# Optimization experiments

Measured on AMD Instinct MI355X. Metric: run time of the kernel, lower is better.

The kernel has to match this reference:

```python
import jax, jax.numpy as jnp
import numpy as np

CLAMP = 2.0
SPLIT1 = 48  # split_len1 (channels - channels//2)


def _down(x):
    # pixel-unshuffle: equivalent to the grouped stride-2 conv with 0/1 kernels
    B, C, H, W = x.shape
    x = x.reshape(B, C, H // 2, 2, W // 2, 2)
    x = x.transpose(0, 1, 3, 5, 2, 4)  # (B, C, di, dj, H/2, W/2)
    return x.reshape(B, C * 4, H // 2, W // 2)


def _conv(x, w, b, stride):
    y = jax.lax.conv_general_dilated(
        x, w, window_strides=(stride, stride), padding=[(1, 1), (1, 1)],
        dimension_numbers=('NCHW', 'OIHW', 'NCHW'))
    return y + b[None, :, None, None]


def _affine(x, a):
    # forward affine coupling: x * exp(clamp*tanh(0.2*a_s)) + a_t
    ch = x.shape[1]
    sub_jac = CLAMP * jnp.tanh(0.2 * a[:, :ch])
    return x * jnp.exp(sub_jac) + a[:, ch:]


def setup_inputs() -> dict:
    key = jax.random.key(0)
    ks = jax.random.split(key, 4)
    B, C, H, W = 32, 96, 64, 64
    s1, s2 = SPLIT1, C - SPLIT1
    x = jax.random.normal(ks[0], (B, C, H, W), jnp.float32)
    # s_hi: strided 3x3 conv, split_len1 -> 8*split_len2
    w_hi = jax.random.normal(ks[1], (8 * s2, s1, 3, 3), jnp.float32) * 0.05
    b_hi = jnp.zeros((8 * s2,), jnp.float32)
    # s_lo: same-res 3x3 conv, 4*split_len2 -> 8*split_len1
    w_lo = jax.random.normal(ks[2], (8 * s1, 4 * s2, 3, 3), jnp.float32) * 0.05
    b_lo = jnp.zeros((8 * s1,), jnp.float32)
    # actnorm params: act_norm init = 10.0 * 1.0 (SOFTPLUS branch)
    ch4 = 4 * C
    act_norm = jnp.full((1, ch4, 1, 1), 10.0, jnp.float32)
    act_offset = jnp.zeros((1, ch4, 1, 1), jnp.float32)
    # hard permutation matrix (permute_soft=False), fixed seed
    rng = np.random.default_rng(0)
    perm = rng.permutation(ch4)
    pw = np.zeros((ch4, ch4), np.float32)
    pw[np.arange(ch4), perm] = 1.0
    perm_w = jnp.asarray(pw)
    return dict(x=x, w_hi=w_hi, b_hi=b_hi, w_lo=w_lo, b_lo=b_lo,
                act_norm=act_norm, act_offset=act_offset, perm_w=perm_w)


def reference(x, w_hi, b_hi, w_lo, b_lo, act_norm, act_offset, perm_w):
    x1, x2 = x[:, :SPLIT1], x[:, SPLIT1:]
    y2 = _down(x2)                     # (B, 4*s2, H/2, W/2)
    a1 = _conv(x1, w_hi, b_hi, 2)      # (B, 8*s2, H/2, W/2)
    y2 = _affine(y2, a1)
    y1 = _down(x1)                     # (B, 4*s1, H/2, W/2)
    a2 = _conv(y2, w_lo, b_lo, 1)      # (B, 8*s1, H/2, W/2)
    y1 = _affine(y1, a2)
    out = jnp.concatenate([y1, y2], axis=1)  # (B, 4*C, H/2, W/2)
    # actnorm (SOFTPLUS: 0.1 * softplus_{beta=0.5}) + hard 1x1 permutation
    scale = 0.2 * jax.nn.softplus(0.5 * act_norm)
    out = jnp.einsum('bchw,oc->bohw', out * scale + act_offset, perm_w)
    return out
```

## Files before the change

kernel.cpp:

```cpp
#include <hip/hip_runtime.h>
#include <hip/hip_bf16.h>

typedef __attribute__((ext_vector_type(8))) short s16x8;
typedef __attribute__((ext_vector_type(4))) short s16x4;
typedef __attribute__((ext_vector_type(4))) float f32x4;
typedef unsigned short u16;

#define WS_FWD    0
#define WS_INV    2048
#define WS_SCALE  4096
#define WS_OFFS   6144
#define WS_WHI    8192
#define WS_XD     2097152
#define WS_WLO    14680064
#define WS_Y2     16777216

static __device__ __forceinline__ u16 f2bf(float f) {
    __hip_bfloat16 h = __float2bfloat16(f);
    return *reinterpret_cast<u16*>(&h);
}
static __device__ __forceinline__ float bf2f(u16 u) {
    __hip_bfloat16 h = *reinterpret_cast<__hip_bfloat16*>(&u);
    return __bfloat162float(h);
}

static __device__ __forceinline__ void gl_lds16(const void* g, void* l) {
    __builtin_amdgcn_global_load_lds(
        (const __attribute__((address_space(1))) unsigned int*)g,
        (__attribute__((address_space(3))) unsigned int*)l, 16, 0, 0);
}


__global__ __launch_bounds__(256)
void k_setup(const float* __restrict__ pw, const float* __restrict__ an,
             const float* __restrict__ ao, const float* __restrict__ w_hi,
             const float* __restrict__ w_lo, int* __restrict__ fwd,
             int* __restrict__ inv, float* __restrict__ scale,
             float* __restrict__ offs, u16* __restrict__ whi,
             u16* __restrict__ wlo)
{
    const int blk = blockIdx.x;
    const int tid = threadIdx.x;
    if (blk < 2592) {
        int gid = blk * 256 + tid;
        int c32 = gid & 31;
        int n   = (gid >> 5) % 384;
        int tkc = gid / (384 * 32);
        int kc  = tkc % 6;
        int t   = tkc / 6;
        int c   = kc * 32 + c32;
        wlo[gid] = f2bf(w_lo[((size_t)n * 192 + c) * 9 + t]);
    } else if (blk < 3744) {
        int gid = (blk - 2592) * 256 + tid;
        int c32 = gid & 31;
        int n   = (gid >> 5) % 384;
        int tkc = gid / (384 * 32);
        int kc  = tkc % 6;
        int t   = tkc / 6;
        int c   = kc * 32 + c32;
        int th = t >> 1, tw = t & 1;
        int cin = c >> 2, dy = (c >> 1) & 1, dx = c & 1;
        float wv = 0.f;
        if (!(th == 0 && dy == 0) && !(tw == 0 && dx == 0)) {
            int ky = (th == 0) ? 0 : 1 + dy;
            int kx = (tw == 0) ? 0 : 1 + dx;
            wv = w_hi[(((size_t)n * 48 + cin) * 3 + ky) * 3 + kx];
        }
        whi[gid] = f2bf(wv);
    } else {
        int gid = (blk - 3744) * 256 + tid;
        int o = gid / 384;
        int c = gid - o * 384;
        if (pw[gid] > 0.5f) { fwd[o] = c; inv[c] = o; }
        if (gid < 384) {
            scale[gid] = 0.2f * log1pf(expf(0.5f * an[gid]));
            offs[gid]  = ao[gid];
        }
    }
}

__global__ __launch_bounds__(256)
void k_xd(const float* __restrict__ x, u16* __restrict__ xd)
{
    int gid = blockIdx.x * 256 + threadIdx.x;
    int pix = gid / 48;
    int j = gid - pix * 48;
    int b = pix >> 10, h = (pix >> 5) & 31, w = pix & 31;
    const float* xp = &x[(((size_t)b * 96 + j) * 64 + 2 * h) * 64 + 2 * w];
    float2 r0 = *(const float2*)xp;
    float2 r1 = *(const float2*)(xp + 64);
    int c0 = j * 4;
    int g = c0 >> 3;
    size_t off = ((size_t)b * 32 + h) * 6144 + w * 192 + ((g ^ (w & 7)) << 3) + (c0 & 7);
    s16x4 v;
    v[0] = (short)f2bf(r0.x); v[1] = (short)f2bf(r0.y);
    v[2] = (short)f2bf(r1.x); v[3] = (short)f2bf(r1.y);
    *(s16x4*)&xd[off] = v;
}

template <int T>
__global__ __launch_bounds__(256)
void f_gemm(const u16* __restrict__ in_t, const u16* __restrict__ wpk,
            const float* __restrict__ bias, const float* __restrict__ x,
            const int* __restrict__ inv, const float* __restrict__ scale,
            const float* __restrict__ offs, u16* __restrict__ y2out,
            float* __restrict__ out)
{
    const int tid = threadIdx.x;
    const int lane = tid & 63;
    const int wave = tid >> 6;
    const int l16 = lane & 15;
    const int quad = lane >> 4;
    const int mblk = blockIdx.x;
    const int b = mblk >> 4;
    const int h0 = (mblk & 15) << 1;
    const int n0 = wave * 96;

    __shared__ u16 sm[384 * 68];

    const s16x8 zero8 = {0, 0, 0, 0, 0, 0, 0, 0};
    for (int r = 0; r < 4; ++r) {
        int ih = h0 - 1 + r;
        if (ih >= 0 && ih < 32) {
            const char* gsrc = (const char*)in_t + ((size_t)b * 32 + ih) * 12288;
#pragma unroll
            for (int j = 0; j < 3; ++j) {
                int off = j * 4096 + tid * 16;
                gl_lds16(gsrc + off, (char*)sm + r * 12288 + off);
            }
        } else {
#pragma unroll
            for (int j = 0; j < 3; ++j)
                *(s16x8*)((char*)sm + r * 12288 + j * 4096 + tid * 16) = zero8;
        }
    }
    __syncthreads();

    const f32x4 zero4 = {0.f, 0.f, 0.f, 0.f};
    f32x4 acc[4][6];
#pragma unroll
    for (int a = 0; a < 4; ++a)
#pragma unroll
        for (int c = 0; c < 6; ++c) acc[a][c] = zero4;

    for (int t = 0; t < T; ++t) {
        const int dh = (T == 4) ? ((t >> 1) - 1) : (t / 3 - 1);
        const int dw = (T == 4) ? ((t & 1) - 1) : (t % 3 - 1);
#pragma unroll
        for (int kc = 0; kc < 6; ++kc) {
            const u16* wp = wpk + ((size_t)(t * 6 + kc) * 384) * 32;
            s16x8 bf[6];
#pragma unroll
            for (int ns = 0; ns < 6; ++ns)
                bf[ns] = *(const s16x8*)(wp + (n0 + ns * 16 + l16) * 32 + quad * 8);
            const int g = kc * 4 + quad;
            s16x8 af[4];
#pragma unroll
            for (int ms = 0; ms < 4; ++ms) {
                int m = ms * 16 + l16;
                int r = (m >> 5) + dh + 1;
                int iw = (m & 31) + dw;
                int iwc = iw < 0 ? 0 : (iw > 31 ? 31 : iw);
                s16x8 v = *(const s16x8*)&sm[r * 6144 + iwc * 192 + ((g ^ (iwc & 7)) << 3)];
                if (iw != iwc) v = zero8;
                af[ms] = v;
            }
#pragma unroll
            for (int ms = 0; ms < 4; ++ms)
#pragma unroll
                for (int ns = 0; ns < 6; ++ns)
                    acc[ms][ns] = __builtin_amdgcn_mfma_f32_16x16x32_bf16(
                        af[ms], bf[ns], acc[ms][ns], 0, 0, 0);
        }
    }

    __syncthreads();

#pragma unroll
    for (int ms = 0; ms < 4; ++ms) {
#pragma unroll
        for (int ns = 0; ns < 6; ++ns) {
            int n = n0 + ns * 16 + l16;
            float bv = bias[n];
            s16x4 pk;
#pragma unroll
            for (int r4 = 0; r4 < 4; ++r4)
                pk[r4] = (short)f2bf(acc[ms][ns][r4] + bv);
            *(s16x4*)&sm[n * 68 + ms * 16 + quad * 4] = pk;
        }
    }
    __syncthreads();

    {
        const int m = lane;
        const int h = h0 + (m >> 5);
        const int w = m & 31;
        for (int i = 0; i < 48; ++i) {
            int c = wave * 48 + i;
            float a_s = bf2f(sm[c * 68 + m]);
            float a_o = bf2f(sm[(c + 192) * 68 + m]);
            int cin = (T == 4 ? 48 : 0) + (c >> 2);
            float xv = x[(((size_t)b * 96 + cin) * 64 + (2 * h + ((c >> 1) & 1))) * 64
                         + (2 * w + (c & 1))];
            float e = expf(0.4f * a_s);
            float sj = 2.f - 4.f / (e + 1.f);
            float y = xv * expf(sj) + a_o;
            int cg = (T == 4) ? (192 + c) : c;
            int o = inv[cg];
            if (T == 4) {
                u16 yb = f2bf(y);
                sm[c * 68 + m] = yb;
                out[(((size_t)b * 384 + o) * 32 + h) * 32 + w] =
                    bf2f(yb) * scale[cg] + offs[cg];
            } else {
                out[(((size_t)b * 384 + o) * 32 + h) * 32 + w] =
                    y * scale[cg] + offs[cg];
            }
        }
    }

    if (T == 4) {
        __syncthreads();
        for (int it = 0; it < 6; ++it) {
            int v = it * 256 + tid;
            int m2 = v / 24;
            int c8 = v - m2 * 24;
            int c0 = c8 * 8;
            int h2 = h0 + (m2 >> 5);
            int w2 = m2 & 31;
            s16x8 yv;
#pragma unroll
            for (int j = 0; j < 8; ++j)
                yv[j] = (short)sm[(c0 + j) * 68 + m2];
            size_t off = ((size_t)b * 32 + h2) * 6144 + w2 * 192 + ((c8 ^ (w2 & 7)) << 3);
            *(s16x8*)&y2out[off] = yv;
        }
    }
}

extern "C" void kernel_launch(void* const* d_in, const int* in_sizes, int n_in,
                              void* d_out, int out_size, void* d_ws, size_t ws_size,
                              hipStream_t stream)
{
    const float* x        = (const float*)d_in[0];
    const float* w_hi     = (const float*)d_in[1];
    const float* b_hi     = (const float*)d_in[2];
    const float* w_lo     = (const float*)d_in[3];
    const float* b_lo     = (const float*)d_in[4];
    const float* act_norm = (const float*)d_in[5];
    const float* act_off  = (const float*)d_in[6];
    const float* perm_w   = (const float*)d_in[7];
    float* out = (float*)d_out;
    char* ws = (char*)d_ws;

    int*   fwd   = (int*)(ws + WS_FWD);
    int*   inv   = (int*)(ws + WS_INV);
    float* scale = (float*)(ws + WS_SCALE);
    float* offs  = (float*)(ws + WS_OFFS);
    u16*   whi   = (u16*)(ws + WS_WHI);
    u16*   xd    = (u16*)(ws + WS_XD);
    u16*   wlo   = (u16*)(ws + WS_WLO);
    u16*   y2    = (u16*)(ws + WS_Y2);

    k_setup<<<4320, 256, 0, stream>>>(perm_w, act_norm, act_off, w_hi, w_lo,
                                      fwd, inv, scale, offs, whi, wlo);
    k_xd<<<6144, 256, 0, stream>>>(x, xd);
    f_gemm<4><<<512, 256, 0, stream>>>(xd, whi, b_hi, x, inv, scale, offs, y2, out);
    f_gemm<9><<<512, 256, 0, stream>>>(y2, wlo, b_lo, x, inv, scale, offs, y2, out);
}
```

Measured before the change: 220.3 us.

## Fuse pixel-unshuffle bf16 conversion into first conv GEMM and coalesce weight packing

Removes the separate k_xd kernel that wrote a bf16 pixel-unshuffled copy of x1 to workspace. The first conv GEMM now reads fp32 x directly, converts it to bf16 and writes the swizzled layout into LDS itself. This drops one launch and one global round trip. The weight-packing setup kernel is also restructured so that each thread reads a contiguous 9-tap source row and scatters the taps, which cuts its block count. The trade-off is that staging is now done with per-thread loads and LDS stores instead of async global_load_lds, and the y2 buffer is passed as an unused input pointer.

```diff
diff --git a/kernel.cpp b/kernel.cpp
--- a/kernel.cpp
+++ b/kernel.cpp
@@ -11,7 +11,6 @@
 #define WS_SCALE  4096
 #define WS_OFFS   6144
 #define WS_WHI    8192
-#define WS_XD     2097152
 #define WS_WLO    14680064
 #define WS_Y2     16777216
 
@@ -41,34 +40,35 @@
 {
     const int blk = blockIdx.x;
     const int tid = threadIdx.x;
-    if (blk < 2592) {
+    if (blk < 288) {
         int gid = blk * 256 + tid;
-        int c32 = gid & 31;
-        int n   = (gid >> 5) % 384;
-        int tkc = gid / (384 * 32);
-        int kc  = tkc % 6;
-        int t   = tkc / 6;
-        int c   = kc * 32 + c32;
-        wlo[gid] = f2bf(w_lo[((size_t)n * 192 + c) * 9 + t]);
-    } else if (blk < 3744) {
-        int gid = (blk - 2592) * 256 + tid;
-        int c32 = gid & 31;
-        int n   = (gid >> 5) % 384;
-        int tkc = gid / (384 * 32);
-        int kc  = tkc % 6;
-        int t   = tkc / 6;
-        int c   = kc * 32 + c32;
-        int th = t >> 1, tw = t & 1;
+        int n = gid / 192;
+        int c = gid - n * 192;
+        int kc = c >> 5, c32 = c & 31;
+        const float* src = w_lo + (size_t)gid * 9;
+#pragma unroll
+        for (int t = 0; t < 9; ++t)
+            wlo[((size_t)(t * 6 + kc) * 384 + n) * 32 + c32] = f2bf(src[t]);
+    } else if (blk < 576) {
+        int gid = (blk - 288) * 256 + tid;
+        int n = gid / 192;
+        int c = gid - n * 192;
+        int kc = c >> 5, c32 = c & 31;
         int cin = c >> 2, dy = (c >> 1) & 1, dx = c & 1;
-        float wv = 0.f;
-        if (!(th == 0 && dy == 0) && !(tw == 0 && dx == 0)) {
-            int ky = (th == 0) ? 0 : 1 + dy;
-            int kx = (tw == 0) ? 0 : 1 + dx;
-            wv = w_hi[(((size_t)n * 48 + cin) * 3 + ky) * 3 + kx];
-        }
-        whi[gid] = f2bf(wv);
+        const float* src = w_hi + ((size_t)n * 48 + cin) * 9;
+#pragma unroll
+        for (int t = 0; t < 4; ++t) {
+            int th = t >> 1, tw = t & 1;
+            float wv = 0.f;
+            if (!(th == 0 && dy == 0) && !(tw == 0 && dx == 0)) {
+                int ky = (th == 0) ? 0 : 1 + dy;
+                int kx = (tw == 0) ? 0 : 1 + dx;
+                wv = src[ky * 3 + kx];
+            }
+            whi[((size_t)(t * 6 + kc) * 384 + n) * 32 + c32] = f2bf(wv);
+        }
     } else {
-        int gid = (blk - 3744) * 256 + tid;
+        int gid = (blk - 576) * 256 + tid;
         int o = gid / 384;
         int c = gid - o * 384;
         if (pw[gid] > 0.5f) { fwd[o] = c; inv[c] = o; }
@@ -77,25 +77,6 @@
             offs[gid]  = ao[gid];
         }
     }
-}
-
-__global__ __launch_bounds__(256)
-void k_xd(const float* __restrict__ x, u16* __restrict__ xd)
-{
-    int gid = blockIdx.x * 256 + threadIdx.x;
-    int pix = gid / 48;
-    int j = gid - pix * 48;
-    int b = pix >> 10, h = (pix >> 5) & 31, w = pix & 31;
-    const float* xp = &x[(((size_t)b * 96 + j) * 64 + 2 * h) * 64 + 2 * w];
-    float2 r0 = *(const float2*)xp;
-    float2 r1 = *(const float2*)(xp + 64);
-    int c0 = j * 4;
-    int g = c0 >> 3;
-    size_t off = ((size_t)b * 32 + h) * 6144 + w * 192 + ((g ^ (w & 7)) << 3) + (c0 & 7);
-    s16x4 v;
-    v[0] = (short)f2bf(r0.x); v[1] = (short)f2bf(r0.y);
-    v[2] = (short)f2bf(r1.x); v[3] = (short)f2bf(r1.y);
-    *(s16x4*)&xd[off] = v;
 }
 
 template <int T>
@@ -119,19 +100,48 @@
     __shared__ u16 sm[384 * 68];
 
     const s16x8 zero8 = {0, 0, 0, 0, 0, 0, 0, 0};
-    for (int r = 0; r < 4; ++r) {
-        int ih = h0 - 1 + r;
-        if (ih >= 0 && ih < 32) {
-            const char* gsrc = (const char*)in_t + ((size_t)b * 32 + ih) * 12288;
-#pragma unroll
-            for (int j = 0; j < 3; ++j) {
-                int off = j * 4096 + tid * 16;
-                gl_lds16(gsrc + off, (char*)sm + r * 12288 + off);
-            }
-        } else {
-#pragma unroll
-            for (int j = 0; j < 3; ++j)
-                *(s16x8*)((char*)sm + r * 12288 + j * 4096 + tid * 16) = zero8;
+
+    if (T == 4) {
+        for (int r = 0; r < 4; ++r) {
+            int ih = h0 - 1 + r;
+            if (ih >= 0 && ih < 32) {
+#pragma unroll
+                for (int it = 0; it < 6; ++it) {
+                    int k = it * 256 + tid;
+                    int cin = k >> 5;
+                    int dy = (k >> 4) & 1;
+                    int q = k & 15;
+                    f32x4 v = *(const f32x4*)&x[((size_t)(b * 96 + cin) * 64
+                                                 + (2 * ih + dy)) * 64 + q * 4];
+                    int ce = cin * 4 + dy * 2;
+                    int g = ce >> 3;
+                    int w0 = 2 * q, w1 = w0 + 1;
+                    unsigned p0 = (unsigned)f2bf(v[0]) | ((unsigned)f2bf(v[1]) << 16);
+                    unsigned p1 = (unsigned)f2bf(v[2]) | ((unsigned)f2bf(v[3]) << 16);
+                    *(unsigned*)&sm[r * 6144 + w0 * 192 + ((g ^ (w0 & 7)) << 3) + (ce & 7)] = p0;
+                    *(unsigned*)&sm[r * 6144 + w1 * 192 + ((g ^ (w1 & 7)) << 3) + (ce & 7)] = p1;
+                }
+            } else {
+#pragma unroll
+                for (int z = 0; z < 12; ++z)
+                    ((unsigned*)&sm[r * 6144])[z * 256 + tid] = 0u;
+            }
+        }
+    } else {
+        for (int r = 0; r < 4; ++r) {
+            int ih = h0 - 1 + r;
+            if (ih >= 0 && ih < 32) {
+                const char* gsrc = (const char*)in_t + ((size_t)b * 32 + ih) * 12288;
+#pragma unroll
+                for (int j = 0; j < 3; ++j) {
+                    int off = j * 4096 + tid * 16;
+                    gl_lds16(gsrc + off, (char*)sm + r * 12288 + off);
+                }
+            } else {
+#pragma unroll
+                for (int j = 0; j < 3; ++j)
+                    *(s16x8*)((char*)sm + r * 12288 + j * 4096 + tid * 16) = zero8;
+            }
         }
     }
     __syncthreads();
@@ -258,13 +268,11 @@
     float* scale = (float*)(ws + WS_SCALE);
     float* offs  = (float*)(ws + WS_OFFS);
     u16*   whi   = (u16*)(ws + WS_WHI);
-    u16*   xd    = (u16*)(ws + WS_XD);
     u16*   wlo   = (u16*)(ws + WS_WLO);
     u16*   y2    = (u16*)(ws + WS_Y2);
 
-    k_setup<<<4320, 256, 0, stream>>>(perm_w, act_norm, act_off, w_hi, w_lo,
+    k_setup<<<1152, 256, 0, stream>>>(perm_w, act_norm, act_off, w_hi, w_lo,
                                       fwd, inv, scale, offs, whi, wlo);
-    k_xd<<<6144, 256, 0, stream>>>(x, xd);
-    f_gemm<4><<<512, 256, 0, stream>>>(xd, whi, b_hi, x, inv, scale, offs, y2, out);
+    f_gemm<4><<<512, 256, 0, stream>>>(y2, whi, b_hi, x, inv, scale, offs, y2, out);
     f_gemm<9><<<512, 256, 0, stream>>>(y2, wlo, b_lo, x, inv, scale, offs, y2, out);
 }
```

Measured after the change: 206.4 us. -6.3%, faster.
